# Kernel optimization log

Hardware: AMD Instinct MI355X
Metric: run time of the kernel (lower is better)

The kernel has to match this reference:

```python
import jax, jax.numpy as jnp
import numpy as np

D_MODEL = 1024
N_HEADS = 16
N_PHASE = 128
HEAD_DIM = D_MODEL // N_HEADS
PHASE_PER_HEAD = N_PHASE // N_HEADS
CONTENT_SCALE = 1.0 / np.sqrt(HEAD_DIM)
PHASE_SCALE = 1.0 / np.sqrt(PHASE_PER_HEAD)
LN_EPS = 1e-5


def create_position_phases(L, n_phase, base=10000.0):
    # RoPE-style: each freq repeated at even/odd indices (interleaved)
    inv_freq = 1.0 / base ** (jnp.arange(0, n_phase, 2, dtype=jnp.float32) / n_phase)
    pos = jnp.arange(L, dtype=jnp.float32)
    sinusoid = pos[:, None] * inv_freq[None, :]          # (L, n_phase//2)
    return jnp.repeat(sinusoid, 2, axis=1)               # (L, n_phase)


def setup_inputs() -> dict:
    key = jax.random.key(0)
    ks = jax.random.split(key, 12)
    B, L, D, P = 1, 2048, D_MODEL, N_PHASE
    s = 0.02
    return {
        'x_real': jax.random.normal(ks[0], (B, L, D), jnp.float32),
        'x_imag': jax.random.normal(ks[1], (B, L, D), jnp.float32),
        'Wq': jax.random.normal(ks[2], (D, D), jnp.float32) * s,
        'Wk': jax.random.normal(ks[3], (D, D), jnp.float32) * s,
        'Wv': jax.random.normal(ks[4], (D, D), jnp.float32) * s,
        'Wqp': jax.random.normal(ks[5], (D, P), jnp.float32) * s,
        'bqp': jax.random.uniform(ks[6], (P,), jnp.float32, -np.pi, np.pi),
        'Wkp': jax.random.normal(ks[7], (D, P), jnp.float32) * s,
        'bkp': jax.random.uniform(ks[8], (P,), jnp.float32, -np.pi, np.pi),
        'Wo': jax.random.normal(ks[9], (D, D), jnp.float32) * s,
        'alpha_logit': jnp.zeros((N_HEADS, 1, 1), jnp.float32),
        'ln_gamma': jnp.ones((D,), jnp.float32),
        'ln_beta': jnp.zeros((D,), jnp.float32),
    }


def _split_heads(x, B, L, H, hd):
    return x.reshape(B, L, H, hd).transpose(0, 2, 1, 3)  # (B,H,L,hd)


def reference(x_real, x_imag, Wq, Wk, Wv, Wqp, bqp, Wkp, bkp, Wo,
              alpha_logit, ln_gamma, ln_beta):
    B, L, D = x_real.shape
    H, hd, p = N_HEADS, HEAD_DIM, PHASE_PER_HEAD

    Q = _split_heads(x_real @ Wq, B, L, H, hd)
    K = _split_heads(x_real @ Wk, B, L, H, hd)
    V = _split_heads(x_real @ Wv, B, L, H, hd)
    content = jnp.einsum('bhqd,bhkd->bhqk', Q, K) * CONTENT_SCALE

    pos_phase = create_position_phases(L, N_PHASE)        # (L, P)
    Qt = _split_heads(x_imag @ Wqp + bqp + pos_phase, B, L, H, p)
    Kt = _split_heads(x_imag @ Wkp + bkp + pos_phase, B, L, H, p)
    phase = (jnp.einsum('bhqp,bhkp->bhqk', jnp.cos(Qt), jnp.cos(Kt))
             + jnp.einsum('bhqp,bhkp->bhqk', jnp.sin(Qt), jnp.sin(Kt))) * PHASE_SCALE

    alpha = jax.nn.sigmoid(alpha_logit)                   # (H,1,1) broadcasts over (B,H,L,L)
    scores = (1.0 - alpha) * content + alpha * phase

    causal = jnp.triu(jnp.ones((L, L), bool), 1)
    scores = jnp.where(causal, -jnp.inf, scores)
    attn = jax.nn.softmax(scores, axis=-1)

    out = jnp.einsum('bhqk,bhkd->bhqd', attn, V)
    out = out.transpose(0, 2, 1, 3).reshape(B, L, D) @ Wo

    h = x_real + out
    mu = jnp.mean(h, axis=-1, keepdims=True)
    var = jnp.var(h, axis=-1, keepdims=True)
    out_real = (h - mu) / jnp.sqrt(var + LN_EPS) * ln_gamma + ln_beta
    return out_real, x_imag
```

## Files before the change

### kernel.cpp

```cpp
#include <hip/hip_runtime.h>
#include <hip/hip_bf16.h>
#include <math.h>

#define L 2048
#define D 1024
#define NH 16
#define HD 64
#define P 128
#define HDE 96
#define CONTENT_SCALE 0.125f
#define PHASE_SCALE   0.35355339059327373f
#define KLS 104
#define VTS 72
#define NSPLIT 2

typedef short bf16x8 __attribute__((ext_vector_type(8)));
typedef float f32x4 __attribute__((ext_vector_type(4)));
typedef float f32x16 __attribute__((ext_vector_type(16)));

__device__ inline ushort f2b(float x) {
    __hip_bfloat16 b = __float2bfloat16(x);
    return *(ushort*)&b;
}
__device__ inline float b2f(ushort u) {
    unsigned v = (unsigned)u << 16;
    union { unsigned u; float f; } c; c.u = v; return c.f;
}

__device__ inline void sincos_hw(float ang, float* sn, float* cs) {
    float rev = ang * 0.15915494309189535f;
    rev -= floorf(rev);
    *sn = __builtin_amdgcn_sinf(rev);
    *cs = __builtin_amdgcn_cosf(rev);
}

__device__ inline void gld_lds16(const void* g, void* l) {
    __builtin_amdgcn_global_load_lds(
        (const __attribute__((address_space(1))) unsigned int*)g,
        (__attribute__((address_space(3))) unsigned int*)l,
        16, 0, 0);
}

__global__ void prep_kernel(const float* __restrict__ xr, const float* __restrict__ xi,
                            ushort* __restrict__ xrb, ushort* __restrict__ xib,
                            const float* __restrict__ W0, const float* __restrict__ W1,
                            const float* __restrict__ W2, const float* __restrict__ W3,
                            const float* __restrict__ W4, const float* __restrict__ W5,
                            ushort* __restrict__ T0, ushort* __restrict__ T1,
                            ushort* __restrict__ T2, ushort* __restrict__ T3,
                            ushort* __restrict__ Tp,
                            ushort* __restrict__ Qe, ushort* __restrict__ Ke) {
    __shared__ float tile[32][33];
    const int b = blockIdx.x;
    const int tid = threadIdx.x;
    if (b < 4096) {
        const float4* src = (b >> 11) ? (const float4*)xi : (const float4*)xr;
        ushort4* dst = (b >> 11) ? (ushort4*)xib : (ushort4*)xrb;
        int i = ((b & 2047) << 8) + tid;
        float4 v = src[i];
        ushort4 o;
        o.x = f2b(v.x); o.y = f2b(v.y); o.z = f2b(v.z); o.w = f2b(v.w);
        dst[i] = o;
    } else if (b < 8448) {
        int w = b - 4096;
        const float* W; ushort* T; int ncols, n0, k0;
        if (w < 4096) {
            int z = w >> 10, t = w & 1023;
            n0 = (t & 31) * 32; k0 = (t >> 5) * 32; ncols = D;
            W = (z == 0) ? W0 : ((z == 1) ? W1 : ((z == 2) ? W2 : W3));
            T = (z == 0) ? T0 : ((z == 1) ? T1 : ((z == 2) ? T2 : T3));
        } else {
            int w2 = w - 4096;
            int z = w2 >> 7, t = w2 & 127;
            n0 = (t & 3) * 32; k0 = (t >> 2) * 32; ncols = P;
            W = z ? W5 : W4;
            T = Tp + (size_t)z * P * D;
        }
        int tx = tid & 31, ty = tid >> 5;
#pragma unroll
        for (int i = 0; i < 4; i++)
            tile[ty + i * 8][tx] = W[(size_t)(k0 + ty + i * 8) * ncols + n0 + tx];
        __syncthreads();
#pragma unroll
        for (int i = 0; i < 4; i++)
            T[(size_t)(n0 + ty + i * 8) * D + k0 + tx] = f2b(tile[tx][ty + i * 8]);
    } else {
        int i = (b - 8448) * 256 + tid;
        size_t base = (size_t)i * HDE + 80;
        uint4 z4 = make_uint4(0, 0, 0, 0);
        *(uint4*)(Qe + base) = z4;
        *(uint4*)(Qe + base + 8) = z4;
        *(uint4*)(Ke + base) = z4;
        *(uint4*)(Ke + base + 8) = z4;
    }
}

__launch_bounds__(256)
__global__ void qkv_gemm(const ushort* __restrict__ Ab, const ushort* __restrict__ xib,
                         const ushort* __restrict__ Wtq, const ushort* __restrict__ Wtk,
                         const ushort* __restrict__ Wtv, const ushort* __restrict__ Wtp,
                         ushort* __restrict__ Qe, ushort* __restrict__ Ke,
                         ushort* __restrict__ Ve, const float* __restrict__ alpha,
                         const float* __restrict__ bqp, const float* __restrict__ bkp) {
    const int z = blockIdx.z;
    if (z == 3 && blockIdx.x >= 2) return;
    const ushort* At = (z == 3) ? xib : Ab;
    const ushort* Bt = (z == 0) ? Wtq : ((z == 1) ? Wtk : ((z == 2) ? Wtv : Wtp));
    __shared__ ushort As[128 * 32];
    __shared__ ushort Bs[128 * 32];
    const int tid = threadIdx.x;
    const int wave = tid >> 6, lane = tid & 63, quad = lane >> 4, ln16 = lane & 15;
    const int wm = wave >> 1, wn = wave & 1;
    const int m0 = blockIdx.y * 128, n0 = blockIdx.x * 128;
    f32x4 acc[4][4];
#pragma unroll
    for (int i = 0; i < 4; i++)
#pragma unroll
        for (int j = 0; j < 4; j++) acc[i][j] = (f32x4){0.f, 0.f, 0.f, 0.f};
    for (int kt = 0; kt < D; kt += 32) {
        __syncthreads();
#pragma unroll
        for (int i = 0; i < 2; i++) {
            int idx = i * 256 + tid;
            int row = idx >> 2, c8 = idx & 3;
            gld_lds16(At + (size_t)(m0 + row) * D + kt + c8 * 8, &As[idx * 8]);
            gld_lds16(Bt + (size_t)(n0 + row) * D + kt + c8 * 8, &Bs[idx * 8]);
        }
        __syncthreads();
        bf16x8 af[4], bfr[4];
#pragma unroll
        for (int t = 0; t < 4; t++) {
            af[t]  = *(const bf16x8*)(&As[(wm * 64 + t * 16 + ln16) * 32 + quad * 8]);
            bfr[t] = *(const bf16x8*)(&Bs[(wn * 64 + t * 16 + ln16) * 32 + quad * 8]);
        }
#pragma unroll
        for (int i = 0; i < 4; i++)
#pragma unroll
            for (int j = 0; j < 4; j++)
                acc[i][j] = __builtin_amdgcn_mfma_f32_16x16x32_bf16(af[i], bfr[j], acc[i][j], 0, 0, 0);
    }
    if (z == 2) {
        int hn = (n0 + wn * 64) >> 6;
#pragma unroll
        for (int i = 0; i < 4; i++)
#pragma unroll
            for (int j = 0; j < 4; j++) {
                int d = j * 16 + ln16;
                int m = m0 + wm * 64 + i * 16 + quad * 4;
                ushort4 pk;
                pk.x = f2b(acc[i][j][0]); pk.y = f2b(acc[i][j][1]);
                pk.z = f2b(acc[i][j][2]); pk.w = f2b(acc[i][j][3]);
                *(ushort4*)(Ve + ((size_t)hn * HD + d) * L + m) = pk;
            }
    } else if (z < 2) {
        int hn = (n0 + wn * 64) >> 6;
        float s = (z == 0) ? (1.f - 1.f / (1.f + __expf(-alpha[hn]))) * CONTENT_SCALE : 1.f;
        ushort* dst = (z == 0) ? Qe : Ke;
#pragma unroll
        for (int i = 0; i < 4; i++)
#pragma unroll
            for (int j = 0; j < 4; j++) {
                int dcol = j * 16 + ln16;
#pragma unroll
                for (int r = 0; r < 4; r++) {
                    int m = m0 + wm * 64 + i * 16 + quad * 4 + r;
                    dst[((size_t)hn * L + m) * HDE + dcol] = f2b(acc[i][j][r] * s);
                }
            }
    } else {
#pragma unroll
        for (int j = 0; j < 4; j++) {
            int cg = n0 + wn * 64 + j * 16 + ln16;
            int isQ = cg < P;
            int c = cg & (P - 1);
            int hh = c >> 3, jj = c & 7;
            float b = isQ ? bqp[c] : bkp[c];
            float sc = isQ ? (1.f / (1.f + __expf(-alpha[hh]))) * PHASE_SCALE : 1.f;
            float invf = __expf(-((float)(c & ~1) / 128.f) * 9.210340371976184f);
            ushort* dst = isQ ? Qe : Ke;
#pragma unroll
            for (int i = 0; i < 4; i++)
#pragma unroll
                for (int r = 0; r < 4; r++) {
                    int m = m0 + wm * 64 + i * 16 + quad * 4 + r;
                    float qt = acc[i][j][r] + b + (float)m * invf;
                    float sn, cs;
                    sincos_hw(qt, &sn, &cs);
                    size_t base = ((size_t)hh * L + m) * HDE;
                    dst[base + 64 + jj] = f2b(sc * cs);
                    dst[base + 72 + jj] = f2b(sc * sn);
                }
        }
    }
}

__launch_bounds__(256, 2)
__global__ void flash_attn(const ushort* __restrict__ Qe, const ushort* __restrict__ Ke,
                           const ushort* __restrict__ Vte,
                           ushort* __restrict__ Opart, float* __restrict__ ml) {
    const int b = blockIdx.x;
    const int xcd = b & 7;
    const int r = b >> 3;
    const int idx = r & 31, sub = r >> 5;
    const int hbit = idx >> 4, c0i = idx & 15;
    const int c = sub ? 15 - c0i : c0i;
    const int z = sub;
    const int h = xcd * 2 + hbit;
    const int tid = threadIdx.x;
    const int wave = tid >> 6, lane = tid & 63;
    const int ln32 = lane & 31, hf = lane >> 5;

    const int nT = c + 1;
    const int s0 = z * nT;
    const int qw = c * 128 + wave * 32;

    __shared__ ushort Kl[64 * KLS];
    __shared__ ushort Vt[64 * VTS];

    const ushort* Kh = Ke + (size_t)h * L * HDE;
    const ushort* Vh = Vte + (size_t)h * HD * L;
    const ushort* Qh = Qe + (size_t)h * L * HDE;
    ushort* Op = Opart + (size_t)z * L * D;
    float* mlp = ml + (size_t)z * NH * L + (size_t)h * L;

    bf16x8 qa[6];
#pragma unroll
    for (int cc = 0; cc < 6; cc++)
        qa[cc] = *(const bf16x8*)(Qh + (size_t)(qw + ln32) * HDE + cc * 16 + hf * 8);

    f32x16 o[2];
#pragma unroll
    for (int i = 0; i < 16; i++) { o[0][i] = 0.f; o[1][i] = 0.f; }
    float olacc = 0.f;

    int rowk[3], colk[3];
#pragma unroll
    for (int ii = 0; ii < 3; ii++) {
        int ix = ii * 256 + tid;
        rowk[ii] = ix / 12; colk[ii] = ix - rowk[ii] * 12;
    }
    int dv[2], cv[2];
#pragma unroll
    for (int ii = 0; ii < 2; ii++) {
        int ix = ii * 256 + tid;
        dv[ii] = ix >> 3; cv[ii] = ix & 7;
    }

    bf16x8 kreg[3], vreg[2];
    {
        int k0 = s0 * 64;
#pragma unroll
        for (int ii = 0; ii < 3; ii++)
            kreg[ii] = *(const bf16x8*)(Kh + (size_t)(k0 + rowk[ii]) * HDE + colk[ii] * 8);
#pragma unroll
        for (int ii = 0; ii < 2; ii++)
            vreg[ii] = *(const bf16x8*)(Vh + (size_t)dv[ii] * L + k0 + cv[ii] * 8);
    }

    for (int t = s0; t < s0 + nT; t++) {
        const int k0 = t * 64;
        __syncthreads();
#pragma unroll
        for (int ii = 0; ii < 3; ii++)
            *(bf16x8*)(&Kl[rowk[ii] * KLS + colk[ii] * 8]) = kreg[ii];
#pragma unroll
        for (int ii = 0; ii < 2; ii++)
            *(bf16x8*)(&Vt[dv[ii] * VTS + cv[ii] * 8]) = vreg[ii];
        __syncthreads();

        if (t + 1 < s0 + nT) {
            int k0n = k0 + 64;
#pragma unroll
            for (int ii = 0; ii < 3; ii++)
                kreg[ii] = *(const bf16x8*)(Kh + (size_t)(k0n + rowk[ii]) * HDE + colk[ii] * 8);
#pragma unroll
            for (int ii = 0; ii < 2; ii++)
                vreg[ii] = *(const bf16x8*)(Vh + (size_t)dv[ii] * L + k0n + cv[ii] * 8);
        }

        if (k0 < qw + 32) {
            f32x16 s2[2];
#pragma unroll
            for (int i = 0; i < 16; i++) { s2[0][i] = 0.f; s2[1][i] = 0.f; }
#pragma unroll
            for (int kb = 0; kb < 2; kb++)
#pragma unroll
                for (int cc = 0; cc < 6; cc++) {
                    bf16x8 kf = *(const bf16x8*)(&Kl[(kb * 32 + ln32) * KLS + cc * 16 + hf * 8]);
                    s2[kb] = __builtin_amdgcn_mfma_f32_32x32x16_bf16(kf, qa[cc], s2[kb], 0, 0, 0);
                }

            if (k0 + 63 > qw) {
#pragma unroll
                for (int kb = 0; kb < 2; kb++)
#pragma unroll
                    for (int rg = 0; rg < 16; rg++) {
                        int key = k0 + kb * 32 + (rg & 3) + 8 * (rg >> 2) + 4 * hf;
                        if (key > qw + ln32) s2[kb][rg] = -1e30f;
                    }
            }

            float p[2][16];
#pragma unroll
            for (int kb = 0; kb < 2; kb++)
#pragma unroll
                for (int rg = 0; rg < 16; rg++) {
                    p[kb][rg] = __expf(s2[kb][rg]);
                    olacc += p[kb][rg];
                }

            unsigned Xp[2][4], Yp[2][4];
#pragma unroll
            for (int kb = 0; kb < 2; kb++)
#pragma unroll
                for (int tq = 0; tq < 4; tq++) {
                    asm("v_cvt_pk_bf16_f32 %0, %1, %2"
                        : "=v"(Xp[kb][tq]) : "v"(p[kb][4 * tq + 0]), "v"(p[kb][4 * tq + 1]));
                    asm("v_cvt_pk_bf16_f32 %0, %1, %2"
                        : "=v"(Yp[kb][tq]) : "v"(p[kb][4 * tq + 2]), "v"(p[kb][4 * tq + 3]));
                }

            bf16x8 pa[4];
#pragma unroll
            for (int m = 0; m < 4; m++) {
                int kb = m >> 1, te = 2 * (m & 1), to = te + 1;
                unsigned x0 = Xp[kb][te], x1 = Xp[kb][to];
                unsigned y0 = Yp[kb][te], y1 = Yp[kb][to];
                asm("v_permlane32_swap_b32 %0, %1" : "+v"(x0), "+v"(x1));
                asm("v_permlane32_swap_b32 %0, %1" : "+v"(y0), "+v"(y1));
                union { unsigned u[4]; bf16x8 v; } pb;
                pb.u[0] = x0; pb.u[1] = y0; pb.u[2] = x1; pb.u[3] = y1;
                pa[m] = pb.v;
            }

#pragma unroll
            for (int m = 0; m < 4; m++)
#pragma unroll
                for (int db = 0; db < 2; db++) {
                    bf16x8 vf = *(const bf16x8*)(&Vt[(db * 32 + ln32) * VTS + m * 16 + hf * 8]);
                    o[db] = __builtin_amdgcn_mfma_f32_32x32x16_bf16(pa[m], vf, o[db], 0, 0, 0);
                }
        }
    }

    {
        union { float f; unsigned u; } a, b2;
        a.f = olacc; b2.f = olacc;
        asm("v_permlane32_swap_b32 %0, %1" : "+v"(a.u), "+v"(b2.u));
        float tot = a.f + b2.f;
        if (lane < 32) mlp[qw + ln32] = tot;
    }
#pragma unroll
    for (int db = 0; db < 2; db++)
#pragma unroll
        for (int rg = 0; rg < 16; rg++) {
            int q = qw + (rg & 3) + 8 * (rg >> 2) + 4 * hf;
            Op[(size_t)q * D + h * HD + db * 32 + ln32] = f2b(o[db][rg]);
        }
}

__global__ void comb_kernel(const ushort* __restrict__ Opart, const float* __restrict__ ml,
                            ushort* __restrict__ AOb) {
    int q = blockIdx.x;
    int t = threadIdx.x;
    int h = t >> 4;
    float lsum = 0.f;
#pragma unroll
    for (int zz = 0; zz < NSPLIT; zz++)
        lsum += ml[(size_t)zz * NH * L + (size_t)h * L + q];
    float inv = 1.f / lsum;
    size_t idx = (size_t)q * D + t * 4;
    float ox = 0.f, oy = 0.f, oz = 0.f, ow = 0.f;
#pragma unroll
    for (int zz = 0; zz < NSPLIT; zz++) {
        ushort4 a = *(const ushort4*)(Opart + (size_t)zz * L * D + idx);
        ox += b2f(a.x); oy += b2f(a.y); oz += b2f(a.z); ow += b2f(a.w);
    }
    ushort4 o;
    o.x = f2b(ox * inv); o.y = f2b(oy * inv);
    o.z = f2b(oz * inv); o.w = f2b(ow * inv);
    *(ushort4*)(AOb + idx) = o;
}

__launch_bounds__(256)
__global__ void wo_gemm(const ushort* __restrict__ Ab, const ushort* __restrict__ Bt,
                        float* __restrict__ C) {
    __shared__ ushort As[128 * 32];
    __shared__ ushort Bs[128 * 32];
    const int tid = threadIdx.x;
    const int wave = tid >> 6, lane = tid & 63, quad = lane >> 4, ln16 = lane & 15;
    const int wm = wave >> 1, wn = wave & 1;
    const int m0 = blockIdx.y * 128, n0 = blockIdx.x * 128;
    f32x4 acc[4][4];
#pragma unroll
    for (int i = 0; i < 4; i++)
#pragma unroll
        for (int j = 0; j < 4; j++) acc[i][j] = (f32x4){0.f, 0.f, 0.f, 0.f};
    for (int kt = 0; kt < D; kt += 32) {
        __syncthreads();
#pragma unroll
        for (int i = 0; i < 2; i++) {
            int idx = i * 256 + tid;
            int row = idx >> 2, c8 = idx & 3;
            gld_lds16(Ab + (size_t)(m0 + row) * D + kt + c8 * 8, &As[idx * 8]);
            gld_lds16(Bt + (size_t)(n0 + row) * D + kt + c8 * 8, &Bs[idx * 8]);
        }
        __syncthreads();
        bf16x8 af[4], bfr[4];
#pragma unroll
        for (int t = 0; t < 4; t++) {
            af[t]  = *(const bf16x8*)(&As[(wm * 64 + t * 16 + ln16) * 32 + quad * 8]);
            bfr[t] = *(const bf16x8*)(&Bs[(wn * 64 + t * 16 + ln16) * 32 + quad * 8]);
        }
#pragma unroll
        for (int i = 0; i < 4; i++)
#pragma unroll
            for (int j = 0; j < 4; j++)
                acc[i][j] = __builtin_amdgcn_mfma_f32_16x16x32_bf16(af[i], bfr[j], acc[i][j], 0, 0, 0);
    }
#pragma unroll
    for (int i = 0; i < 4; i++)
#pragma unroll
        for (int j = 0; j < 4; j++)
#pragma unroll
            for (int r = 0; r < 4; r++) {
                int m = m0 + wm * 64 + i * 16 + quad * 4 + r;
                int n = n0 + wn * 64 + j * 16 + ln16;
                C[(size_t)m * D + n] = acc[i][j][r];
            }
}

__global__ void ln_kernel(const float* __restrict__ xr, const float* __restrict__ o2,
                          const float* __restrict__ gamma, const float* __restrict__ beta,
                          float* __restrict__ outp, const float4* __restrict__ xi4,
                          float4* __restrict__ out1) {
    int l = blockIdx.x;
    int tid = threadIdx.x;
    int wave = tid >> 6;
    __shared__ float red[8];
    float hv[4];
    float s = 0.f;
#pragma unroll
    for (int i = 0; i < 4; i++) {
        int c = tid + i * 256;
        hv[i] = xr[(size_t)l * D + c] + o2[(size_t)l * D + c];
        s += hv[i];
    }
    out1[(size_t)l * (D / 4) + tid] = xi4[(size_t)l * (D / 4) + tid];
#pragma unroll
    for (int off = 1; off < 64; off <<= 1) s += __shfl_xor(s, off);
    if ((tid & 63) == 0) red[wave] = s;
    __syncthreads();
    float mu = (red[0] + red[1] + red[2] + red[3]) * (1.f / D);
    float v = 0.f;
#pragma unroll
    for (int i = 0; i < 4; i++) { float d = hv[i] - mu; v += d * d; }
#pragma unroll
    for (int off = 1; off < 64; off <<= 1) v += __shfl_xor(v, off);
    __syncthreads();
    if ((tid & 63) == 0) red[4 + wave] = v;
    __syncthreads();
    float rstd = rsqrtf((red[4] + red[5] + red[6] + red[7]) * (1.f / D) + 1e-5f);
#pragma unroll
    for (int i = 0; i < 4; i++) {
        int c = tid + i * 256;
        outp[(size_t)l * D + c] = (hv[i] - mu) * rstd * gamma[c] + beta[c];
    }
}

extern "C" void kernel_launch(void* const* d_in, const int* in_sizes, int n_in,
                              void* d_out, int out_size, void* d_ws, size_t ws_size,
                              hipStream_t stream) {
    const float* xr    = (const float*)d_in[0];
    const float* xi    = (const float*)d_in[1];
    const float* Wq    = (const float*)d_in[2];
    const float* Wk    = (const float*)d_in[3];
    const float* Wv    = (const float*)d_in[4];
    const float* Wqp   = (const float*)d_in[5];
    const float* bqp   = (const float*)d_in[6];
    const float* Wkp   = (const float*)d_in[7];
    const float* bkp   = (const float*)d_in[8];
    const float* Wo    = (const float*)d_in[9];
    const float* alpha = (const float*)d_in[10];
    const float* gamma = (const float*)d_in[11];
    const float* beta  = (const float*)d_in[12];

    const size_t LD = (size_t)L * D;
    const size_t MB = 1024 * 1024;

    char* A8 = (char*)d_out;
    char* B8 = A8 + LD * 4;
    ushort* xib = (ushort*)A8;
    ushort* AOb = (ushort*)A8;
    ushort* Wot = (ushort*)(A8 + 4 * MB);
    ushort* Wtq = (ushort*)(A8 + 6 * MB);
    ushort* xrb = (ushort*)B8;
    ushort* Wtk = (ushort*)(B8 + 4 * MB);
    ushort* Wtv = (ushort*)(B8 + 6 * MB);
    float* outf = (float*)d_out;

    ushort* Qe = (ushort*)d_ws;
    ushort* Ke = Qe + (size_t)NH * L * HDE;
    ushort* Ve = Ke + (size_t)NH * L * HDE;
    ushort* Wqpkt = Ve + (size_t)NH * L * HD;
    ushort* Opart = Wqpkt + (size_t)256 * D;
    float*  mlbuf = (float*)(Opart + (size_t)NSPLIT * LD);
    float*  O2 = (float*)d_ws;

    prep_kernel<<<8576, 256, 0, stream>>>(xr, xi, xrb, xib,
                                          Wq, Wk, Wv, Wo, Wqp, Wkp,
                                          Wtq, Wtk, Wtv, Wot, Wqpkt, Qe, Ke);

    qkv_gemm<<<dim3(8, 16, 4), 256, 0, stream>>>(xrb, xib, Wtq, Wtk, Wtv, Wqpkt,
                                                 Qe, Ke, Ve, alpha, bqp, bkp);

    flash_attn<<<512, 256, 0, stream>>>(Qe, Ke, Ve, Opart, mlbuf);

    comb_kernel<<<L, 256, 0, stream>>>(Opart, mlbuf, AOb);

    wo_gemm<<<dim3(8, 16), 256, 0, stream>>>(AOb, Wot, O2);

    ln_kernel<<<L, 256, 0, stream>>>(xr, O2, gamma, beta, outf,
                                     (const float4*)xi, (float4*)(B8));
}
```

Baseline: 190.8 us.

## Double-buffer LDS tiles in projection GEMMs and raise MFMA priority in attention

The QKV and output-projection GEMMs now use two LDS buffers per operand. The next K-tile's global-to-LDS loads are issued before the MFMAs on the current tile, and each iteration ends with a single barrier instead of two. In the attention kernel, s_setprio is raised around the QK^T and PV MFMA blocks so that waves issuing matrix work get scheduling priority over waves doing softmax. The cost is twice the LDS per GEMM block, which may reduce occupancy, and the priority hints may not help on every scheduling pattern.

```diff
diff --git a/kernel.cpp b/kernel.cpp
--- a/kernel.cpp
+++ b/kernel.cpp
@@ -106,39 +106,55 @@
     if (z == 3 && blockIdx.x >= 2) return;
     const ushort* At = (z == 3) ? xib : Ab;
     const ushort* Bt = (z == 0) ? Wtq : ((z == 1) ? Wtk : ((z == 2) ? Wtv : Wtp));
-    __shared__ ushort As[128 * 32];
-    __shared__ ushort Bs[128 * 32];
+    __shared__ ushort As[2][128 * 32];
+    __shared__ ushort Bs[2][128 * 32];
     const int tid = threadIdx.x;
     const int wave = tid >> 6, lane = tid & 63, quad = lane >> 4, ln16 = lane & 15;
     const int wm = wave >> 1, wn = wave & 1;
     const int m0 = blockIdx.y * 128, n0 = blockIdx.x * 128;
+    const int row = tid >> 2, c8 = tid & 3;
     f32x4 acc[4][4];
 #pragma unroll
     for (int i = 0; i < 4; i++)
 #pragma unroll
         for (int j = 0; j < 4; j++) acc[i][j] = (f32x4){0.f, 0.f, 0.f, 0.f};
+
+#pragma unroll
+    for (int i = 0; i < 2; i++) {
+        int idx = i * 256 + tid;
+        int r2 = idx >> 2, cc = idx & 3;
+        gld_lds16(At + (size_t)(m0 + r2) * D + cc * 8, &As[0][idx * 8]);
+        gld_lds16(Bt + (size_t)(n0 + r2) * D + cc * 8, &Bs[0][idx * 8]);
+    }
+    __syncthreads();
+
+    int cur = 0;
     for (int kt = 0; kt < D; kt += 32) {
-        __syncthreads();
-#pragma unroll
-        for (int i = 0; i < 2; i++) {
-            int idx = i * 256 + tid;
-            int row = idx >> 2, c8 = idx & 3;
-            gld_lds16(At + (size_t)(m0 + row) * D + kt + c8 * 8, &As[idx * 8]);
-            gld_lds16(Bt + (size_t)(n0 + row) * D + kt + c8 * 8, &Bs[idx * 8]);
-        }
-        __syncthreads();
+        if (kt + 32 < D) {
+#pragma unroll
+            for (int i = 0; i < 2; i++) {
+                int idx = i * 256 + tid;
+                int r2 = idx >> 2, cc = idx & 3;
+                gld_lds16(At + (size_t)(m0 + r2) * D + kt + 32 + cc * 8, &As[cur ^ 1][idx * 8]);
+                gld_lds16(Bt + (size_t)(n0 + r2) * D + kt + 32 + cc * 8, &Bs[cur ^ 1][idx * 8]);
+            }
+        }
         bf16x8 af[4], bfr[4];
 #pragma unroll
         for (int t = 0; t < 4; t++) {
-            af[t]  = *(const bf16x8*)(&As[(wm * 64 + t * 16 + ln16) * 32 + quad * 8]);
-            bfr[t] = *(const bf16x8*)(&Bs[(wn * 64 + t * 16 + ln16) * 32 + quad * 8]);
+            af[t]  = *(const bf16x8*)(&As[cur][(wm * 64 + t * 16 + ln16) * 32 + quad * 8]);
+            bfr[t] = *(const bf16x8*)(&Bs[cur][(wn * 64 + t * 16 + ln16) * 32 + quad * 8]);
         }
 #pragma unroll
         for (int i = 0; i < 4; i++)
 #pragma unroll
             for (int j = 0; j < 4; j++)
                 acc[i][j] = __builtin_amdgcn_mfma_f32_16x16x32_bf16(af[i], bfr[j], acc[i][j], 0, 0, 0);
-    }
+        __syncthreads();
+        cur ^= 1;
+    }
+    (void)row; (void)c8;
+
     if (z == 2) {
         int hn = (n0 + wn * 64) >> 6;
 #pragma unroll
@@ -282,6 +298,7 @@
             f32x16 s2[2];
 #pragma unroll
             for (int i = 0; i < 16; i++) { s2[0][i] = 0.f; s2[1][i] = 0.f; }
+            __builtin_amdgcn_s_setprio(1);
 #pragma unroll
             for (int kb = 0; kb < 2; kb++)
 #pragma unroll
@@ -289,6 +306,7 @@
                     bf16x8 kf = *(const bf16x8*)(&Kl[(kb * 32 + ln32) * KLS + cc * 16 + hf * 8]);
                     s2[kb] = __builtin_amdgcn_mfma_f32_32x32x16_bf16(kf, qa[cc], s2[kb], 0, 0, 0);
                 }
+            __builtin_amdgcn_s_setprio(0);
 
             if (k0 + 63 > qw) {
 #pragma unroll
@@ -333,6 +351,7 @@
                 pa[m] = pb.v;
             }
 
+            __builtin_amdgcn_s_setprio(1);
 #pragma unroll
             for (int m = 0; m < 4; m++)
 #pragma unroll
@@ -340,6 +359,7 @@
                     bf16x8 vf = *(const bf16x8*)(&Vt[(db * 32 + ln32) * VTS + m * 16 + hf * 8]);
                     o[db] = __builtin_amdgcn_mfma_f32_32x32x16_bf16(pa[m], vf, o[db], 0, 0, 0);
                 }
+            __builtin_amdgcn_s_setprio(0);
         }
     }
 
@@ -385,8 +405,8 @@
 __launch_bounds__(256)
 __global__ void wo_gemm(const ushort* __restrict__ Ab, const ushort* __restrict__ Bt,
                         float* __restrict__ C) {
-    __shared__ ushort As[128 * 32];
-    __shared__ ushort Bs[128 * 32];
+    __shared__ ushort As[2][128 * 32];
+    __shared__ ushort Bs[2][128 * 32];
     const int tid = threadIdx.x;
     const int wave = tid >> 6, lane = tid & 63, quad = lane >> 4, ln16 = lane & 15;
     const int wm = wave >> 1, wn = wave & 1;
@@ -396,27 +416,40 @@
     for (int i = 0; i < 4; i++)
 #pragma unroll
         for (int j = 0; j < 4; j++) acc[i][j] = (f32x4){0.f, 0.f, 0.f, 0.f};
+
+#pragma unroll
+    for (int i = 0; i < 2; i++) {
+        int idx = i * 256 + tid;
+        int r2 = idx >> 2, cc = idx & 3;
+        gld_lds16(Ab + (size_t)(m0 + r2) * D + cc * 8, &As[0][idx * 8]);
+        gld_lds16(Bt + (size_t)(n0 + r2) * D + cc * 8, &Bs[0][idx * 8]);
+    }
+    __syncthreads();
+
+    int cur = 0;
     for (int kt = 0; kt < D; kt += 32) {
-        __syncthreads();
-#pragma unroll
-        for (int i = 0; i < 2; i++) {
-            int idx = i * 256 + tid;
-            int row = idx >> 2, c8 = idx & 3;
-            gld_lds16(Ab + (size_t)(m0 + row) * D + kt + c8 * 8, &As[idx * 8]);
-            gld_lds16(Bt + (size_t)(n0 + row) * D + kt + c8 * 8, &Bs[idx * 8]);
-        }
-        __syncthreads();
+        if (kt + 32 < D) {
+#pragma unroll
+            for (int i = 0; i < 2; i++) {
+                int idx = i * 256 + tid;
+                int r2 = idx >> 2, cc = idx & 3;
+                gld_lds16(Ab + (size_t)(m0 + r2) * D + kt + 32 + cc * 8, &As[cur ^ 1][idx * 8]);
+                gld_lds16(Bt + (size_t)(n0 + r2) * D + kt + 32 + cc * 8, &Bs[cur ^ 1][idx * 8]);
+            }
+        }
         bf16x8 af[4], bfr[4];
 #pragma unroll
         for (int t = 0; t < 4; t++) {
-            af[t]  = *(const bf16x8*)(&As[(wm * 64 + t * 16 + ln16) * 32 + quad * 8]);
-            bfr[t] = *(const bf16x8*)(&Bs[(wn * 64 + t * 16 + ln16) * 32 + quad * 8]);
+            af[t]  = *(const bf16x8*)(&As[cur][(wm * 64 + t * 16 + ln16) * 32 + quad * 8]);
+            bfr[t] = *(const bf16x8*)(&Bs[cur][(wn * 64 + t * 16 + ln16) * 32 + quad * 8]);
         }
 #pragma unroll
         for (int i = 0; i < 4; i++)
 #pragma unroll
             for (int j = 0; j < 4; j++)
                 acc[i][j] = __builtin_amdgcn_mfma_f32_16x16x32_bf16(af[i], bfr[j], acc[i][j], 0, 0, 0);
+        __syncthreads();
+        cur ^= 1;
     }
 #pragma unroll
     for (int i = 0; i < 4; i++)
```

New measurement: 189.7 us. Within noise of the previous version (-0.6%).

## Double-buffer GEMM LDS tiles and process 128-key chunks in flash attention

Applied to the files above, without the earlier changes.

The QKV and output-projection GEMMs now use two LDS buffers, so the global-to-LDS copy of the next K slice is issued before computing on the current one, and the loop waits at one barrier per slice instead of two. Flash attention stages 128 keys of K and V per barrier instead of 64, which halves the number of synchronizations. It also computes the softmax row sums with an extra MFMA against a vector of ones rather than scalar adds, and raises wave priority around the MFMA blocks. The trade-offs are more LDS per block, which may lower occupancy, extra prefetch registers, and row sums accumulated from bf16-rounded probabilities.

```diff
diff --git a/kernel.cpp b/kernel.cpp
--- a/kernel.cpp
+++ b/kernel.cpp
@@ -11,7 +11,7 @@
 #define CONTENT_SCALE 0.125f
 #define PHASE_SCALE   0.35355339059327373f
 #define KLS 104
-#define VTS 72
+#define VT2 136
 #define NSPLIT 2
 
 typedef short bf16x8 __attribute__((ext_vector_type(8)));
@@ -106,8 +106,8 @@
     if (z == 3 && blockIdx.x >= 2) return;
     const ushort* At = (z == 3) ? xib : Ab;
     const ushort* Bt = (z == 0) ? Wtq : ((z == 1) ? Wtk : ((z == 2) ? Wtv : Wtp));
-    __shared__ ushort As[128 * 32];
-    __shared__ ushort Bs[128 * 32];
+    __shared__ ushort As0[128 * 32], Bs0[128 * 32];
+    __shared__ ushort As1[128 * 32], Bs1[128 * 32];
     const int tid = threadIdx.x;
     const int wave = tid >> 6, lane = tid & 63, quad = lane >> 4, ln16 = lane & 15;
     const int wm = wave >> 1, wn = wave & 1;
@@ -117,28 +117,41 @@
     for (int i = 0; i < 4; i++)
 #pragma unroll
         for (int j = 0; j < 4; j++) acc[i][j] = (f32x4){0.f, 0.f, 0.f, 0.f};
-    for (int kt = 0; kt < D; kt += 32) {
-        __syncthreads();
+
+    auto stage = [&](int kt, ushort* Asb, ushort* Bsb) {
 #pragma unroll
         for (int i = 0; i < 2; i++) {
             int idx = i * 256 + tid;
-            int row = idx >> 2, c8 = idx & 3;
-            gld_lds16(At + (size_t)(m0 + row) * D + kt + c8 * 8, &As[idx * 8]);
-            gld_lds16(Bt + (size_t)(n0 + row) * D + kt + c8 * 8, &Bs[idx * 8]);
-        }
-        __syncthreads();
+            int r2 = idx >> 2, cc = idx & 3;
+            gld_lds16(At + (size_t)(m0 + r2) * D + kt + cc * 8, &Asb[idx * 8]);
+            gld_lds16(Bt + (size_t)(n0 + r2) * D + kt + cc * 8, &Bsb[idx * 8]);
+        }
+    };
+    auto compute = [&](const ushort* Asb, const ushort* Bsb) {
         bf16x8 af[4], bfr[4];
 #pragma unroll
         for (int t = 0; t < 4; t++) {
-            af[t]  = *(const bf16x8*)(&As[(wm * 64 + t * 16 + ln16) * 32 + quad * 8]);
-            bfr[t] = *(const bf16x8*)(&Bs[(wn * 64 + t * 16 + ln16) * 32 + quad * 8]);
+            af[t]  = *(const bf16x8*)(&Asb[(wm * 64 + t * 16 + ln16) * 32 + quad * 8]);
+            bfr[t] = *(const bf16x8*)(&Bsb[(wn * 64 + t * 16 + ln16) * 32 + quad * 8]);
         }
 #pragma unroll
         for (int i = 0; i < 4; i++)
 #pragma unroll
             for (int j = 0; j < 4; j++)
                 acc[i][j] = __builtin_amdgcn_mfma_f32_16x16x32_bf16(af[i], bfr[j], acc[i][j], 0, 0, 0);
-    }
+    };
+
+    stage(0, As0, Bs0);
+    __syncthreads();
+    for (int kt = 0; kt < D; kt += 64) {
+        stage(kt + 32, As1, Bs1);
+        compute(As0, Bs0);
+        __syncthreads();
+        if (kt + 64 < D) stage(kt + 64, As0, Bs0);
+        compute(As1, Bs1);
+        __syncthreads();
+    }
+
     if (z == 2) {
         int hn = (n0 + wn * 64) >> 6;
 #pragma unroll
@@ -212,10 +225,11 @@
 
     const int nT = c + 1;
     const int s0 = z * nT;
+    const int nR = (nT + 1) >> 1;
     const int qw = c * 128 + wave * 32;
 
-    __shared__ ushort Kl[64 * KLS];
-    __shared__ ushort Vt[64 * VTS];
+    __shared__ ushort Kl[128 * KLS];
+    __shared__ ushort Vt[64 * VT2];
 
     const ushort* Kh = Ke + (size_t)h * L * HDE;
     const ushort* Vh = Vte + (size_t)h * HD * L;
@@ -223,132 +237,143 @@
     ushort* Op = Opart + (size_t)z * L * D;
     float* mlp = ml + (size_t)z * NH * L + (size_t)h * L;
 
+    bf16x8 onesv;
+#pragma unroll
+    for (int i = 0; i < 8; i++) onesv[i] = (short)0x3F80;
+
     bf16x8 qa[6];
 #pragma unroll
     for (int cc = 0; cc < 6; cc++)
         qa[cc] = *(const bf16x8*)(Qh + (size_t)(qw + ln32) * HDE + cc * 16 + hf * 8);
 
-    f32x16 o[2];
-#pragma unroll
-    for (int i = 0; i < 16; i++) { o[0][i] = 0.f; o[1][i] = 0.f; }
-    float olacc = 0.f;
-
-    int rowk[3], colk[3];
-#pragma unroll
-    for (int ii = 0; ii < 3; ii++) {
+    f32x16 o[2], olv;
+#pragma unroll
+    for (int i = 0; i < 16; i++) { o[0][i] = 0.f; o[1][i] = 0.f; olv[i] = 0.f; }
+
+    int rowk[6], colk[6];
+#pragma unroll
+    for (int ii = 0; ii < 6; ii++) {
         int ix = ii * 256 + tid;
         rowk[ii] = ix / 12; colk[ii] = ix - rowk[ii] * 12;
     }
-    int dv[2], cv[2];
-#pragma unroll
-    for (int ii = 0; ii < 2; ii++) {
+    int dv[4], cv[4];
+#pragma unroll
+    for (int ii = 0; ii < 4; ii++) {
         int ix = ii * 256 + tid;
-        dv[ii] = ix >> 3; cv[ii] = ix & 7;
-    }
-
-    bf16x8 kreg[3], vreg[2];
+        dv[ii] = ix >> 4; cv[ii] = ix & 15;
+    }
+
+    bf16x8 kreg[6], vreg[4];
     {
-        int k0 = s0 * 64;
-#pragma unroll
-        for (int ii = 0; ii < 3; ii++)
-            kreg[ii] = *(const bf16x8*)(Kh + (size_t)(k0 + rowk[ii]) * HDE + colk[ii] * 8);
-#pragma unroll
-        for (int ii = 0; ii < 2; ii++)
-            vreg[ii] = *(const bf16x8*)(Vh + (size_t)dv[ii] * L + k0 + cv[ii] * 8);
-    }
-
-    for (int t = s0; t < s0 + nT; t++) {
-        const int k0 = t * 64;
-        __syncthreads();
-#pragma unroll
-        for (int ii = 0; ii < 3; ii++)
+        int kk = s0 * 64;
+#pragma unroll
+        for (int ii = 0; ii < 6; ii++)
+            kreg[ii] = *(const bf16x8*)(Kh + (size_t)(kk + rowk[ii]) * HDE + colk[ii] * 8);
+#pragma unroll
+        for (int ii = 0; ii < 4; ii++)
+            vreg[ii] = *(const bf16x8*)(Vh + (size_t)dv[ii] * L + kk + cv[ii] * 8);
+    }
+
+    for (int rr = 0; rr < nR; rr++) {
+        const int tk0 = (s0 + rr * 2) * 64;
+        __syncthreads();
+#pragma unroll
+        for (int ii = 0; ii < 6; ii++)
             *(bf16x8*)(&Kl[rowk[ii] * KLS + colk[ii] * 8]) = kreg[ii];
 #pragma unroll
-        for (int ii = 0; ii < 2; ii++)
-            *(bf16x8*)(&Vt[dv[ii] * VTS + cv[ii] * 8]) = vreg[ii];
-        __syncthreads();
-
-        if (t + 1 < s0 + nT) {
-            int k0n = k0 + 64;
-#pragma unroll
-            for (int ii = 0; ii < 3; ii++)
-                kreg[ii] = *(const bf16x8*)(Kh + (size_t)(k0n + rowk[ii]) * HDE + colk[ii] * 8);
-#pragma unroll
-            for (int ii = 0; ii < 2; ii++)
-                vreg[ii] = *(const bf16x8*)(Vh + (size_t)dv[ii] * L + k0n + cv[ii] * 8);
-        }
-
-        if (k0 < qw + 32) {
-            f32x16 s2[2];
-#pragma unroll
-            for (int i = 0; i < 16; i++) { s2[0][i] = 0.f; s2[1][i] = 0.f; }
-#pragma unroll
-            for (int kb = 0; kb < 2; kb++)
-#pragma unroll
-                for (int cc = 0; cc < 6; cc++) {
-                    bf16x8 kf = *(const bf16x8*)(&Kl[(kb * 32 + ln32) * KLS + cc * 16 + hf * 8]);
-                    s2[kb] = __builtin_amdgcn_mfma_f32_32x32x16_bf16(kf, qa[cc], s2[kb], 0, 0, 0);
+        for (int ii = 0; ii < 4; ii++)
+            *(bf16x8*)(&Vt[dv[ii] * VT2 + cv[ii] * 8]) = vreg[ii];
+        __syncthreads();
+
+        if (rr + 1 < nR) {
+            int kk = tk0 + 128;
+#pragma unroll
+            for (int ii = 0; ii < 6; ii++)
+                kreg[ii] = *(const bf16x8*)(Kh + (size_t)(kk + rowk[ii]) * HDE + colk[ii] * 8);
+#pragma unroll
+            for (int ii = 0; ii < 4; ii++)
+                vreg[ii] = *(const bf16x8*)(Vh + (size_t)dv[ii] * L + kk + cv[ii] * 8);
+        }
+
+#pragma unroll
+        for (int hb = 0; hb < 2; hb++) {
+            const int tt = rr * 2 + hb;
+            const int k0 = tk0 + hb * 64;
+            if (tt < nT && k0 < qw + 32) {
+                f32x16 s2[2];
+#pragma unroll
+                for (int i = 0; i < 16; i++) { s2[0][i] = 0.f; s2[1][i] = 0.f; }
+                __builtin_amdgcn_s_setprio(1);
+#pragma unroll
+                for (int kb = 0; kb < 2; kb++)
+#pragma unroll
+                    for (int cc = 0; cc < 6; cc++) {
+                        bf16x8 kf = *(const bf16x8*)(&Kl[(hb * 64 + kb * 32 + ln32) * KLS + cc * 16 + hf * 8]);
+                        s2[kb] = __builtin_amdgcn_mfma_f32_32x32x16_bf16(kf, qa[cc], s2[kb], 0, 0, 0);
+                    }
+                __builtin_amdgcn_s_setprio(0);
+
+                if (k0 + 63 > qw) {
+#pragma unroll
+                    for (int kb = 0; kb < 2; kb++)
+#pragma unroll
+                        for (int rg = 0; rg < 16; rg++) {
+                            int key = k0 + kb * 32 + (rg & 3) + 8 * (rg >> 2) + 4 * hf;
+                            if (key > qw + ln32) s2[kb][rg] = -1e30f;
+                        }
                 }
 
-            if (k0 + 63 > qw) {
 #pragma unroll
                 for (int kb = 0; kb < 2; kb++)
 #pragma unroll
-                    for (int rg = 0; rg < 16; rg++) {
-                        int key = k0 + kb * 32 + (rg & 3) + 8 * (rg >> 2) + 4 * hf;
-                        if (key > qw + ln32) s2[kb][rg] = -1e30f;
+                    for (int rg = 0; rg < 16; rg++)
+                        s2[kb][rg] = __expf(s2[kb][rg]);
+
+                unsigned Xp[2][4], Yp[2][4];
+#pragma unroll
+                for (int kb = 0; kb < 2; kb++)
+#pragma unroll
+                    for (int tq = 0; tq < 4; tq++) {
+                        asm("v_cvt_pk_bf16_f32 %0, %1, %2"
+                            : "=v"(Xp[kb][tq]) : "v"(s2[kb][4 * tq + 0]), "v"(s2[kb][4 * tq + 1]));
+                        asm("v_cvt_pk_bf16_f32 %0, %1, %2"
+                            : "=v"(Yp[kb][tq]) : "v"(s2[kb][4 * tq + 2]), "v"(s2[kb][4 * tq + 3]));
                     }
+
+                bf16x8 pa[4];
+#pragma unroll
+                for (int m = 0; m < 4; m++) {
+                    int kb = m >> 1, te = 2 * (m & 1), to = te + 1;
+                    unsigned x0 = Xp[kb][te], x1 = Xp[kb][to];
+                    unsigned y0 = Yp[kb][te], y1 = Yp[kb][to];
+                    asm("v_permlane32_swap_b32 %0, %1" : "+v"(x0), "+v"(x1));
+                    asm("v_permlane32_swap_b32 %0, %1" : "+v"(y0), "+v"(y1));
+                    union { unsigned u[4]; bf16x8 v; } pb;
+                    pb.u[0] = x0; pb.u[1] = y0; pb.u[2] = x1; pb.u[3] = y1;
+                    pa[m] = pb.v;
+                }
+
+                __builtin_amdgcn_s_setprio(1);
+#pragma unroll
+                for (int m = 0; m < 4; m++) {
+#pragma unroll
+                    for (int db = 0; db < 2; db++) {
+                        bf16x8 vf = *(const bf16x8*)(&Vt[(db * 32 + ln32) * VT2 + hb * 64 + m * 16 + hf * 8]);
+                        o[db] = __builtin_amdgcn_mfma_f32_32x32x16_bf16(pa[m], vf, o[db], 0, 0, 0);
+                    }
+                    olv = __builtin_amdgcn_mfma_f32_32x32x16_bf16(pa[m], onesv, olv, 0, 0, 0);
+                }
+                __builtin_amdgcn_s_setprio(0);
             }
-
-            float p[2][16];
-#pragma unroll
-            for (int kb = 0; kb < 2; kb++)
-#pragma unroll
-                for (int rg = 0; rg < 16; rg++) {
-                    p[kb][rg] = __expf(s2[kb][rg]);
-                    olacc += p[kb][rg];
-                }
-
-            unsigned Xp[2][4], Yp[2][4];
-#pragma unroll
-            for (int kb = 0; kb < 2; kb++)
-#pragma unroll
-                for (int tq = 0; tq < 4; tq++) {
-                    asm("v_cvt_pk_bf16_f32 %0, %1, %2"
-                        : "=v"(Xp[kb][tq]) : "v"(p[kb][4 * tq + 0]), "v"(p[kb][4 * tq + 1]));
-                    asm("v_cvt_pk_bf16_f32 %0, %1, %2"
-                        : "=v"(Yp[kb][tq]) : "v"(p[kb][4 * tq + 2]), "v"(p[kb][4 * tq + 3]));
-                }
-
-            bf16x8 pa[4];
-#pragma unroll
-            for (int m = 0; m < 4; m++) {
-                int kb = m >> 1, te = 2 * (m & 1), to = te + 1;
-                unsigned x0 = Xp[kb][te], x1 = Xp[kb][to];
-                unsigned y0 = Yp[kb][te], y1 = Yp[kb][to];
-                asm("v_permlane32_swap_b32 %0, %1" : "+v"(x0), "+v"(x1));
-                asm("v_permlane32_swap_b32 %0, %1" : "+v"(y0), "+v"(y1));
-                union { unsigned u[4]; bf16x8 v; } pb;
-                pb.u[0] = x0; pb.u[1] = y0; pb.u[2] = x1; pb.u[3] = y1;
-                pa[m] = pb.v;
-            }
-
-#pragma unroll
-            for (int m = 0; m < 4; m++)
-#pragma unroll
-                for (int db = 0; db < 2; db++) {
-                    bf16x8 vf = *(const bf16x8*)(&Vt[(db * 32 + ln32) * VTS + m * 16 + hf * 8]);
-                    o[db] = __builtin_amdgcn_mfma_f32_32x32x16_bf16(pa[m], vf, o[db], 0, 0, 0);
-                }
-        }
-    }
-
-    {
-        union { float f; unsigned u; } a, b2;
-        a.f = olacc; b2.f = olacc;
-        asm("v_permlane32_swap_b32 %0, %1" : "+v"(a.u), "+v"(b2.u));
-        float tot = a.f + b2.f;
-        if (lane < 32) mlp[qw + ln32] = tot;
+        }
+    }
+
+    if (ln32 == 0) {
+#pragma unroll
+        for (int rg = 0; rg < 16; rg++) {
+            int q = qw + (rg & 3) + 8 * (rg >> 2) + 4 * hf;
+            mlp[q] = olv[rg];
+        }
     }
 #pragma unroll
     for (int db = 0; db < 2; db++)
@@ -385,8 +410,8 @@
 __launch_bounds__(256)
 __global__ void wo_gemm(const ushort* __restrict__ Ab, const ushort* __restrict__ Bt,
                         float* __restrict__ C) {
-    __shared__ ushort As[128 * 32];
-    __shared__ ushort Bs[128 * 32];
+    __shared__ ushort As0[128 * 32], Bs0[128 * 32];
+    __shared__ ushort As1[128 * 32], Bs1[128 * 32];
     const int tid = threadIdx.x;
     const int wave = tid >> 6, lane = tid & 63, quad = lane >> 4, ln16 = lane & 15;
     const int wm = wave >> 1, wn = wave & 1;
@@ -396,27 +421,39 @@
     for (int i = 0; i < 4; i++)
 #pragma unroll
         for (int j = 0; j < 4; j++) acc[i][j] = (f32x4){0.f, 0.f, 0.f, 0.f};
-    for (int kt = 0; kt < D; kt += 32) {
-        __syncthreads();
+
+    auto stage = [&](int kt, ushort* Asb, ushort* Bsb) {
 #pragma unroll
         for (int i = 0; i < 2; i++) {
             int idx = i * 256 + tid;
-            int row = idx >> 2, c8 = idx & 3;
-            gld_lds16(Ab + (size_t)(m0 + row) * D + kt + c8 * 8, &As[idx * 8]);
-            gld_lds16(Bt + (size_t)(n0 + row) * D + kt + c8 * 8, &Bs[idx * 8]);
-        }
-        __syncthreads();
+            int r2 = idx >> 2, cc = idx & 3;
+            gld_lds16(Ab + (size_t)(m0 + r2) * D + kt + cc * 8, &Asb[idx * 8]);
+            gld_lds16(Bt + (size_t)(n0 + r2) * D + kt + cc * 8, &Bsb[idx * 8]);
+        }
+    };
+    auto compute = [&](const ushort* Asb, const ushort* Bsb) {
         bf16x8 af[4], bfr[4];
 #pragma unroll
         for (int t = 0; t < 4; t++) {
-            af[t]  = *(const bf16x8*)(&As[(wm * 64 + t * 16 + ln16) * 32 + quad * 8]);
-            bfr[t] = *(const bf16x8*)(&Bs[(wn * 64 + t * 16 + ln16) * 32 + quad * 8]);
+            af[t]  = *(const bf16x8*)(&Asb[(wm * 64 + t * 16 + ln16) * 32 + quad * 8]);
+            bfr[t] = *(const bf16x8*)(&Bsb[(wn * 64 + t * 16 + ln16) * 32 + quad * 8]);
         }
 #pragma unroll
         for (int i = 0; i < 4; i++)
 #pragma unroll
             for (int j = 0; j < 4; j++)
                 acc[i][j] = __builtin_amdgcn_mfma_f32_16x16x32_bf16(af[i], bfr[j], acc[i][j], 0, 0, 0);
+    };
+
+    stage(0, As0, Bs0);
+    __syncthreads();
+    for (int kt = 0; kt < D; kt += 64) {
+        stage(kt + 32, As1, Bs1);
+        compute(As0, Bs0);
+        __syncthreads();
+        if (kt + 64 < D) stage(kt + 64, As0, Bs0);
+        compute(As1, Bs1);
+        __syncthreads();
     }
 #pragma unroll
     for (int i = 0; i < 4; i++)
```

New measurement: 182.8 us. 1.04x faster.
